# Kernel tuning notes

Measured on AMD Instinct MI355X. Metric: run time of the kernel, lower is better.

## Reference

```python
import jax, jax.numpy as jnp
import numpy as np

B = 262144      # Monte Carlo samples (batch)
DH = 128        # d_hidden
DM = 4          # concatenated input feature dim (two one-hot spins)


def _glorot(key, shape):
    fan_in, fan_out = shape[0], shape[1]
    lim = jnp.sqrt(6.0 / (fan_in + fan_out)).astype(jnp.float32)
    return jax.random.uniform(key, shape, jnp.float32, -lim, lim)


def setup_inputs() -> dict:
    key = jax.random.key(0)
    ks = jax.random.split(key, 10)
    inputs = jax.random.normal(ks[0], (B, DM), jnp.float32)
    h1 = jax.random.normal(ks[1], (B, DH), jnp.float32)
    h2 = jax.random.normal(ks[2], (B, DH), jnp.float32)
    U1 = _glorot(ks[3], (DH, DH))
    U2 = _glorot(ks[4], (DH, DH))
    # flax GRUCell params: input kernels (with bias), hidden kernels
    # (r,z: no bias; n: bias). Packed as [ir|iz|in] and [hr|hz].
    Wi = _glorot(ks[5], (DM, 3 * DH))
    bi = jnp.zeros((3 * DH,), jnp.float32)
    Whrz = _glorot(ks[6], (DH, 2 * DH))
    Whn = _glorot(ks[7], (DH, DH))
    bhn = jnp.zeros((DH,), jnp.float32)
    return {"inputs": inputs, "h1": h1, "h2": h2, "U1": U1, "U2": U2,
            "Wi": Wi, "bi": bi, "Whrz": Whrz, "Whn": Whn, "bhn": bhn}


def reference(inputs, h1, h2, U1, U2, Wi, bi, Whrz, Whn, bhn):
    # Fuse the two neighbor hidden states: h = h1 @ U1 + h2 @ U2
    h = h1 @ U1 + h2 @ U2                      # [B, DH]
    # flax GRUCell(carry=h, inputs=x):
    i_proj = inputs @ Wi + bi                  # [B, 3*DH]
    ir, iz, i_n = jnp.split(i_proj, 3, axis=-1)
    hrz = h @ Whrz                             # [B, 2*DH] (no bias in flax)
    hr, hz = jnp.split(hrz, 2, axis=-1)
    r = jax.nn.sigmoid(ir + hr)
    z = jax.nn.sigmoid(iz + hz)
    n = jnp.tanh(i_n + r * (h @ Whn + bhn))
    new_h = (1.0 - z) * n + z * h
    return (new_h, new_h)
```

## Files before the change

kernel.cpp:

```cpp
#include <hip/hip_runtime.h>

using bf8 = __attribute__((ext_vector_type(8))) short;
using bf4 = __attribute__((ext_vector_type(4))) short;
using f4  = __attribute__((ext_vector_type(4))) float;
using u16 = unsigned short;

#define NROWS 262144

#define FLAG_B   0
#define PU_B     128
#define PW2_B    (PU_B + 65536)
#define PWI_B    (PW2_B + 98304)
#define BI_B     (PWI_B + 6144)
#define BHN_B    (BI_B + 1536)

#define PACK_ITEMS 83968

static __device__ __forceinline__ float bf2f(u16 u) {
    unsigned v = ((unsigned)u) << 16;
    return __builtin_bit_cast(float, v);
}
static __device__ __forceinline__ u16 f2bf(float f) {
    unsigned x = __builtin_bit_cast(unsigned, f);
    x = x + 0x7fffu + ((x >> 16) & 1u);
    return (u16)(x >> 16);
}

template<bool FP32>
static __device__ __forceinline__ u16 ldw(const void* p, int i) {
    if constexpr (FP32) return f2bf(((const float*)p)[i]);
    else                return ((const u16*)p)[i];
}
template<bool FP32>
static __device__ __forceinline__ float ldf(const void* p, int i) {
    if constexpr (FP32) return ((const float*)p)[i];
    else                return bf2f(((const u16*)p)[i]);
}
template<bool FP32>
static __device__ __forceinline__ bf8 ld8(const void* base, int idx) {
    if constexpr (!FP32) {
        return *(const bf8*)((const u16*)base + idx);
    } else {
        const float* f = (const float*)base + idx;
        f4 u = *(const f4*)f;
        f4 v = *(const f4*)(f + 4);
        bf8 r;
        r[0]=(short)f2bf(u[0]); r[1]=(short)f2bf(u[1]); r[2]=(short)f2bf(u[2]); r[3]=(short)f2bf(u[3]);
        r[4]=(short)f2bf(v[0]); r[5]=(short)f2bf(v[1]); r[6]=(short)f2bf(v[2]); r[7]=(short)f2bf(v[3]);
        return r;
    }
}
template<bool FP32>
static __device__ __forceinline__ void st8(void* base, int idx, bf8 v) {
    if constexpr (!FP32) {
        *(bf8*)((u16*)base + idx) = v;
    } else {
        float* f = (float*)base + idx;
        f4 a, b;
        a[0]=bf2f((u16)v[0]); a[1]=bf2f((u16)v[1]); a[2]=bf2f((u16)v[2]); a[3]=bf2f((u16)v[3]);
        b[0]=bf2f((u16)v[4]); b[1]=bf2f((u16)v[5]); b[2]=bf2f((u16)v[6]); b[3]=bf2f((u16)v[7]);
        *(f4*)f = a; *(f4*)(f + 4) = b;
    }
}

__global__ void detect_mode(const u16* __restrict__ h1u, int* __restrict__ flag) {
    if (threadIdx.x == 0 && blockIdx.x == 0) {
        int huge = 0;
#pragma unroll 8
        for (int i = 0; i < 256; ++i) {
            u16 v = h1u[i * 2];
            huge += (((v >> 7) & 0xFF) >= 0xC0);
        }
        *flag = (huge > 0) ? 1 : 0;
    }
}

template<bool FP32>
__global__ void prep_pack(const void* __restrict__ U1, const void* __restrict__ U2,
                          const void* __restrict__ Whrz, const void* __restrict__ Whn,
                          const void* __restrict__ Wi, const void* __restrict__ bi,
                          const void* __restrict__ bhn, char* __restrict__ ws,
                          const int* __restrict__ flag)
{
    if ((*flag != 0) != FP32) return;
    int e = blockIdx.x * 256 + threadIdx.x;
    if (e >= PACK_ITEMS) return;
    u16*   pU   = (u16*)(ws + PU_B);
    u16*   pW2  = (u16*)(ws + PW2_B);
    float* wiF  = (float*)(ws + PWI_B);
    float* biF  = (float*)(ws + BI_B);
    float* bhnF = (float*)(ws + BHN_B);
    if (e < 32768) {
        int j = e & 7, lane = (e >> 3) & 63, f = e >> 9;
        int kb = f & 7, nt = f >> 3;
        int k = kb * 32 + (lane >> 4) * 8 + j;
        int n = nt * 16 + (lane & 15);
        pU[e] = (k < 128) ? ldw<FP32>(U1, k * 128 + n) : ldw<FP32>(U2, (k - 128) * 128 + n);
    } else if (e < 81920) {
        int e2 = e - 32768;
        int j = e2 & 7, lane = (e2 >> 3) & 63, f = e2 >> 9;
        int kb = f & 3, nt = f >> 2;
        int k = kb * 32 + (lane >> 4) * 8 + j;
        int n = nt * 16 + (lane & 15);
        pW2[e2] = (n < 256) ? ldw<FP32>(Whrz, k * 256 + n) : ldw<FP32>(Whn, k * 128 + (n - 256));
    } else if (e < 83456) {
        int e3 = e - 81920;
        int k = e3 & 3, c = e3 >> 2;
        wiF[e3] = ldf<FP32>(Wi, k * 384 + c);
    } else if (e < 83840) {
        int i = e - 83456;  biF[i] = ldf<FP32>(bi, i);
    } else {
        int i = e - 83840;  bhnF[i] = ldf<FP32>(bhn, i);
    }
}

template<bool FP32>
__global__ __launch_bounds__(256, 3) void gru_fused(
    const void* __restrict__ xin, const void* __restrict__ h1,
    const void* __restrict__ h2, const char* __restrict__ ws,
    void* __restrict__ out, const int* __restrict__ flag, int write2)
{
    if ((*flag != 0) != FP32) return;
    __shared__ __align__(16) u16 hl[4][32][136];
    const int tid = threadIdx.x;
    const int w  = tid >> 6;
    const int l  = tid & 63;
    const int q  = l >> 4;
    const int lr = l & 15;
    const int g0 = blockIdx.x * 128 + w * 32;

    const bf8* __restrict__ pU  = (const bf8*)(ws + PU_B);
    const bf8* __restrict__ pW2 = (const bf8*)(ws + PW2_B);

    bf8 a[2][8];
#pragma unroll
    for (int m = 0; m < 2; ++m) {
        int row = g0 + m * 16 + lr;
        int base = row * 128 + q * 8;
#pragma unroll
        for (int kb = 0; kb < 4; ++kb) {
            a[m][kb]     = ld8<FP32>(h1, base + kb * 32);
            a[m][kb + 4] = ld8<FP32>(h2, base + kb * 32);
        }
    }
#pragma unroll 1
    for (int nt = 0; nt < 8; ++nt) {
        f4 acc0 = {0.f, 0.f, 0.f, 0.f};
        f4 acc1 = {0.f, 0.f, 0.f, 0.f};
#pragma unroll
        for (int kb = 0; kb < 8; ++kb) {
            bf8 b = pU[(nt * 8 + kb) * 64 + l];
            acc0 = __builtin_amdgcn_mfma_f32_16x16x32_bf16(a[0][kb], b, acc0, 0, 0, 0);
            acc1 = __builtin_amdgcn_mfma_f32_16x16x32_bf16(a[1][kb], b, acc1, 0, 0, 0);
        }
        int col = nt * 16 + lr;
#pragma unroll
        for (int i = 0; i < 4; ++i) {
            hl[w][q * 4 + i][col]      = f2bf(acc0[i]);
            hl[w][16 + q * 4 + i][col] = f2bf(acc1[i]);
        }
    }

    bf8 ah[2][4];
#pragma unroll
    for (int m = 0; m < 2; ++m)
#pragma unroll
        for (int kb = 0; kb < 4; ++kb)
            ah[m][kb] = *(const bf8*)&hl[w][m * 16 + lr][kb * 32 + q * 8];

    float xf[2][4][4];
#pragma unroll
    for (int m = 0; m < 2; ++m)
#pragma unroll
        for (int i = 0; i < 4; ++i) {
            int row = g0 + m * 16 + q * 4 + i;
            if constexpr (FP32) {
                f4 xv = *(const f4*)((const float*)xin + row * 4);
#pragma unroll
                for (int k = 0; k < 4; ++k) xf[m][i][k] = xv[k];
            } else {
                bf4 xv = *(const bf4*)((const u16*)xin + row * 4);
#pragma unroll
                for (int k = 0; k < 4; ++k) xf[m][i][k] = bf2f((u16)xv[k]);
            }
        }

    const float* wiF  = (const float*)(ws + PWI_B);
    const float* biF  = (const float*)(ws + BI_B);
    const float* bhnF = (const float*)(ws + BHN_B);

#pragma unroll 1
    for (int nt = 0; nt < 8; ++nt) {
        f4 aR[2], aZ[2], aN[2];
#pragma unroll
        for (int m = 0; m < 2; ++m) {
            aR[m] = {0.f,0.f,0.f,0.f}; aZ[m] = {0.f,0.f,0.f,0.f}; aN[m] = {0.f,0.f,0.f,0.f};
        }
#pragma unroll
        for (int kb = 0; kb < 4; ++kb) {
            bf8 bR = pW2[((nt     ) * 4 + kb) * 64 + l];
            bf8 bZ = pW2[((nt + 8 ) * 4 + kb) * 64 + l];
            bf8 bN = pW2[((nt + 16) * 4 + kb) * 64 + l];
#pragma unroll
            for (int m = 0; m < 2; ++m) {
                aR[m] = __builtin_amdgcn_mfma_f32_16x16x32_bf16(ah[m][kb], bR, aR[m], 0, 0, 0);
                aZ[m] = __builtin_amdgcn_mfma_f32_16x16x32_bf16(ah[m][kb], bZ, aZ[m], 0, 0, 0);
                aN[m] = __builtin_amdgcn_mfma_f32_16x16x32_bf16(ah[m][kb], bN, aN[m], 0, 0, 0);
            }
        }
        int c = nt * 16 + lr;
        f4 wr = *(const f4*)(wiF + c * 4);
        f4 wz = *(const f4*)(wiF + (128 + c) * 4);
        f4 wn = *(const f4*)(wiF + (256 + c) * 4);
        float bir = biF[c], biz = biF[128 + c], bin = biF[256 + c], bhc = bhnF[c];
#pragma unroll
        for (int m = 0; m < 2; ++m)
#pragma unroll
            for (int i = 0; i < 4; ++i) {
                int rl = m * 16 + q * 4 + i;
                float ir = bir, iz = biz, inn = bin;
#pragma unroll
                for (int k = 0; k < 4; ++k) {
                    ir  = fmaf(xf[m][i][k], wr[k], ir);
                    iz  = fmaf(xf[m][i][k], wz[k], iz);
                    inn = fmaf(xf[m][i][k], wn[k], inn);
                }
                float hv = bf2f(hl[w][rl][c]);
                float sr = ir + aR[m][i];
                sr = fminf(fmaxf(sr, -30.f), 30.f);
                float r = __fdividef(1.f, 1.f + __expf(-sr));
                float sz = iz + aZ[m][i];
                sz = fminf(fmaxf(sz, -30.f), 30.f);
                float z = __fdividef(1.f, 1.f + __expf(-sz));
                float t = inn + r * (aN[m][i] + bhc);
                t = fminf(fmaxf(t, -15.f), 15.f);
                float e2t = __expf(2.f * t);
                float n = (e2t - 1.f) * __fdividef(1.f, e2t + 1.f);
                float o = (1.f - z) * n + z * hv;
                hl[w][rl][c] = f2bf(o);
            }
    }

#pragma unroll
    for (int ii = 0; ii < 8; ++ii) {
        int ch  = ii * 64 + l;
        int row = ch >> 4;
        int c8  = (ch & 15) * 8;
        bf8 v = *(const bf8*)&hl[w][row][c8];
        int off = (g0 + row) * 128 + c8;
        st8<FP32>(out, off, v);
        if (write2) st8<FP32>(out, NROWS * 128 + off, v);
    }
}

extern "C" void kernel_launch(void* const* d_in, const int* in_sizes, int n_in,
                              void* d_out, int out_size, void* d_ws, size_t ws_size,
                              hipStream_t stream) {
    const void* x    = d_in[0];
    const void* h1   = d_in[1];
    const void* h2   = d_in[2];
    const void* U1   = d_in[3];
    const void* U2   = d_in[4];
    const void* Wi   = d_in[5];
    const void* bi   = d_in[6];
    const void* Whrz = d_in[7];
    const void* Whn  = d_in[8];
    const void* bhn  = d_in[9];
    char* ws   = (char*)d_ws;
    int* flag  = (int*)(ws + FLAG_B);
    int write2 = (out_size >= 2 * NROWS * 128) ? 1 : 0;

    detect_mode<<<1, 64, 0, stream>>>((const u16*)h1, flag);
    const int pblk = (PACK_ITEMS + 255) / 256;
    prep_pack<false><<<pblk, 256, 0, stream>>>(U1, U2, Whrz, Whn, Wi, bi, bhn, ws, flag);
    prep_pack<true ><<<pblk, 256, 0, stream>>>(U1, U2, Whrz, Whn, Wi, bi, bhn, ws, flag);
    gru_fused<false><<<NROWS / 128, 256, 0, stream>>>(x, h1, h2, ws, d_out, flag, write2);
    gru_fused<true ><<<NROWS / 128, 256, 0, stream>>>(x, h1, h2, ws, d_out, flag, write2);
}
```

Before: 547.4 us.

## Fold U into hidden GRU weights and compute input projection with MFMA

Precomputes V = [U1;U2] @ [Whrz|Whn] in the pack kernel, so gate pre-activations come straight from [h1|h2] in one K=256 pass, alongside h itself. This removes the LDS round-trip of h and the second dependent GEMM stage. The input projection plus bias is folded into an MFMA with a padded x vector carrying a constant one. Outputs are written directly with nontemporal scalar stores instead of being staged in shared memory. The trade-off is more total MFMA work (K=256 instead of 128 for the gates), less coalesced stores, and different bf16 rounding, since h is no longer rounded before the second product.

Result: slower. 598.4 us (+9.3%).

```diff
diff --git a/kernel.cpp b/kernel.cpp
--- a/kernel.cpp
+++ b/kernel.cpp
@@ -9,12 +9,14 @@
 
 #define FLAG_B   0
 #define PU_B     128
-#define PW2_B    (PU_B + 65536)
-#define PWI_B    (PW2_B + 98304)
-#define BI_B     (PWI_B + 6144)
-#define BHN_B    (BI_B + 1536)
-
-#define PACK_ITEMS 83968
+#define PV_B     (PU_B + 65536)
+#define PWI_B    (PV_B + 196608)
+#define BHN_B    (PWI_B + 24576)
+
+#define N_PU   32768
+#define N_PV   98304
+#define N_PWI  12288
+#define PACK_ITEMS (N_PU + N_PV + N_PWI + 128)
 
 static __device__ __forceinline__ float bf2f(u16 u) {
     unsigned v = ((unsigned)u) << 16;
@@ -50,18 +52,6 @@
         return r;
     }
 }
-template<bool FP32>
-static __device__ __forceinline__ void st8(void* base, int idx, bf8 v) {
-    if constexpr (!FP32) {
-        *(bf8*)((u16*)base + idx) = v;
-    } else {
-        float* f = (float*)base + idx;
-        f4 a, b;
-        a[0]=bf2f((u16)v[0]); a[1]=bf2f((u16)v[1]); a[2]=bf2f((u16)v[2]); a[3]=bf2f((u16)v[3]);
-        b[0]=bf2f((u16)v[4]); b[1]=bf2f((u16)v[5]); b[2]=bf2f((u16)v[6]); b[3]=bf2f((u16)v[7]);
-        *(f4*)f = a; *(f4*)(f + 4) = b;
-    }
-}
 
 __global__ void detect_mode(const u16* __restrict__ h1u, int* __restrict__ flag) {
     if (threadIdx.x == 0 && blockIdx.x == 0) {
@@ -86,31 +76,46 @@
     int e = blockIdx.x * 256 + threadIdx.x;
     if (e >= PACK_ITEMS) return;
     u16*   pU   = (u16*)(ws + PU_B);
-    u16*   pW2  = (u16*)(ws + PW2_B);
-    float* wiF  = (float*)(ws + PWI_B);
-    float* biF  = (float*)(ws + BI_B);
+    u16*   pV   = (u16*)(ws + PV_B);
+    u16*   pWi  = (u16*)(ws + PWI_B);
     float* bhnF = (float*)(ws + BHN_B);
-    if (e < 32768) {
+    if (e < N_PU) {
         int j = e & 7, lane = (e >> 3) & 63, f = e >> 9;
         int kb = f & 7, nt = f >> 3;
         int k = kb * 32 + (lane >> 4) * 8 + j;
         int n = nt * 16 + (lane & 15);
         pU[e] = (k < 128) ? ldw<FP32>(U1, k * 128 + n) : ldw<FP32>(U2, (k - 128) * 128 + n);
-    } else if (e < 81920) {
-        int e2 = e - 32768;
+    } else if (e < N_PU + N_PV) {
+        int e2 = e - N_PU;
         int j = e2 & 7, lane = (e2 >> 3) & 63, f = e2 >> 9;
-        int kb = f & 3, nt = f >> 2;
+        int kb = f & 7, nt = f >> 3;
         int k = kb * 32 + (lane >> 4) * 8 + j;
         int n = nt * 16 + (lane & 15);
-        pW2[e2] = (n < 256) ? ldw<FP32>(Whrz, k * 256 + n) : ldw<FP32>(Whn, k * 128 + (n - 256));
-    } else if (e < 83456) {
-        int e3 = e - 81920;
-        int k = e3 & 3, c = e3 >> 2;
-        wiF[e3] = ldf<FP32>(Wi, k * 384 + c);
-    } else if (e < 83840) {
-        int i = e - 83456;  biF[i] = ldf<FP32>(bi, i);
+        const void* Us = (k < 128) ? U1 : U2;
+        int krow = (k < 128) ? k : k - 128;
+        float acc = 0.f;
+        if (n < 256) {
+#pragma unroll 8
+            for (int j2 = 0; j2 < 128; ++j2)
+                acc = fmaf(ldf<FP32>(Us, krow * 128 + j2), ldf<FP32>(Whrz, j2 * 256 + n), acc);
+        } else {
+#pragma unroll 8
+            for (int j2 = 0; j2 < 128; ++j2)
+                acc = fmaf(ldf<FP32>(Us, krow * 128 + j2), ldf<FP32>(Whn, j2 * 128 + (n - 256)), acc);
+        }
+        pV[e2] = f2bf(acc);
+    } else if (e < N_PU + N_PV + N_PWI) {
+        int e3 = e - (N_PU + N_PV);
+        int j = e3 & 7, lane = (e3 >> 3) & 63, nt = e3 >> 9;
+        int k = (lane >> 4) * 8 + j;
+        int n = nt * 16 + (lane & 15);
+        u16 v = 0;
+        if (k < 4)       v = ldw<FP32>(Wi, k * 384 + n);
+        else if (k == 4) v = ldw<FP32>(bi, n);
+        pWi[e3] = v;
     } else {
-        int i = e - 83840;  bhnF[i] = ldf<FP32>(bhn, i);
+        int i = e - (N_PU + N_PV + N_PWI);
+        bhnF[i] = ldf<FP32>(bhn, i);
     }
 }
 
@@ -121,7 +126,6 @@
     void* __restrict__ out, const int* __restrict__ flag, int write2)
 {
     if ((*flag != 0) != FP32) return;
-    __shared__ __align__(16) u16 hl[4][32][136];
     const int tid = threadIdx.x;
     const int w  = tid >> 6;
     const int l  = tid & 63;
@@ -130,7 +134,9 @@
     const int g0 = blockIdx.x * 128 + w * 32;
 
     const bf8* __restrict__ pU  = (const bf8*)(ws + PU_B);
-    const bf8* __restrict__ pW2 = (const bf8*)(ws + PW2_B);
+    const bf8* __restrict__ pV  = (const bf8*)(ws + PV_B);
+    const bf8* __restrict__ pWi = (const bf8*)(ws + PWI_B);
+    const float* __restrict__ bhnF = (const float*)(ws + BHN_B);
 
     bf8 a[2][8];
 #pragma unroll
@@ -143,113 +149,87 @@
             a[m][kb + 4] = ld8<FP32>(h2, base + kb * 32);
         }
     }
+
+    bf8 ax[2];
+#pragma unroll
+    for (int m = 0; m < 2; ++m) {
+        bf8 v = {0,0,0,0,0,0,0,0};
+        if (q == 0) {
+            int row = g0 + m * 16 + lr;
+            if constexpr (FP32) {
+                f4 xv = *(const f4*)((const float*)xin + row * 4);
+#pragma unroll
+                for (int k = 0; k < 4; ++k) v[k] = (short)f2bf(xv[k]);
+            } else {
+                bf4 xv = *(const bf4*)((const u16*)xin + row * 4);
+#pragma unroll
+                for (int k = 0; k < 4; ++k) v[k] = xv[k];
+            }
+            v[4] = (short)0x3F80;
+        }
+        ax[m] = v;
+    }
+
+    float* outF = (float*)out;
+    u16*   outB = (u16*)out;
+
 #pragma unroll 1
     for (int nt = 0; nt < 8; ++nt) {
-        f4 acc0 = {0.f, 0.f, 0.f, 0.f};
-        f4 acc1 = {0.f, 0.f, 0.f, 0.f};
+        const f4 z4 = {0.f, 0.f, 0.f, 0.f};
+        f4 aH[2], aR[2], aZ[2], aN[2], aI[2];
+        bf8 biR = pWi[(nt     ) * 64 + l];
+        bf8 biZ = pWi[(nt + 8 ) * 64 + l];
+        bf8 biN = pWi[(nt + 16) * 64 + l];
+#pragma unroll
+        for (int m = 0; m < 2; ++m) {
+            aH[m] = z4;
+            aN[m] = z4;
+            aR[m] = __builtin_amdgcn_mfma_f32_16x16x32_bf16(ax[m], biR, z4, 0, 0, 0);
+            aZ[m] = __builtin_amdgcn_mfma_f32_16x16x32_bf16(ax[m], biZ, z4, 0, 0, 0);
+            aI[m] = __builtin_amdgcn_mfma_f32_16x16x32_bf16(ax[m], biN, z4, 0, 0, 0);
+        }
 #pragma unroll
         for (int kb = 0; kb < 8; ++kb) {
-            bf8 b = pU[(nt * 8 + kb) * 64 + l];
-            acc0 = __builtin_amdgcn_mfma_f32_16x16x32_bf16(a[0][kb], b, acc0, 0, 0, 0);
-            acc1 = __builtin_amdgcn_mfma_f32_16x16x32_bf16(a[1][kb], b, acc1, 0, 0, 0);
-        }
-        int col = nt * 16 + lr;
-#pragma unroll
-        for (int i = 0; i < 4; ++i) {
-            hl[w][q * 4 + i][col]      = f2bf(acc0[i]);
-            hl[w][16 + q * 4 + i][col] = f2bf(acc1[i]);
-        }
-    }
-
-    bf8 ah[2][4];
-#pragma unroll
-    for (int m = 0; m < 2; ++m)
-#pragma unroll
-        for (int kb = 0; kb < 4; ++kb)
-            ah[m][kb] = *(const bf8*)&hl[w][m * 16 + lr][kb * 32 + q * 8];
-
-    float xf[2][4][4];
-#pragma unroll
-    for (int m = 0; m < 2; ++m)
-#pragma unroll
-        for (int i = 0; i < 4; ++i) {
-            int row = g0 + m * 16 + q * 4 + i;
-            if constexpr (FP32) {
-                f4 xv = *(const f4*)((const float*)xin + row * 4);
-#pragma unroll
-                for (int k = 0; k < 4; ++k) xf[m][i][k] = xv[k];
-            } else {
-                bf4 xv = *(const bf4*)((const u16*)xin + row * 4);
-#pragma unroll
-                for (int k = 0; k < 4; ++k) xf[m][i][k] = bf2f((u16)xv[k]);
+            bf8 bH = pU[(nt * 8 + kb) * 64 + l];
+            bf8 bR = pV[((nt     ) * 8 + kb) * 64 + l];
+            bf8 bZ = pV[((nt + 8 ) * 8 + kb) * 64 + l];
+            bf8 bN = pV[((nt + 16) * 8 + kb) * 64 + l];
+#pragma unroll
+            for (int m = 0; m < 2; ++m) {
+                aH[m] = __builtin_amdgcn_mfma_f32_16x16x32_bf16(a[m][kb], bH, aH[m], 0, 0, 0);
+                aR[m] = __builtin_amdgcn_mfma_f32_16x16x32_bf16(a[m][kb], bR, aR[m], 0, 0, 0);
+                aZ[m] = __builtin_amdgcn_mfma_f32_16x16x32_bf16(a[m][kb], bZ, aZ[m], 0, 0, 0);
+                aN[m] = __builtin_amdgcn_mfma_f32_16x16x32_bf16(a[m][kb], bN, aN[m], 0, 0, 0);
             }
         }
-
-    const float* wiF  = (const float*)(ws + PWI_B);
-    const float* biF  = (const float*)(ws + BI_B);
-    const float* bhnF = (const float*)(ws + BHN_B);
-
-#pragma unroll 1
-    for (int nt = 0; nt < 8; ++nt) {
-        f4 aR[2], aZ[2], aN[2];
+        int c = nt * 16 + lr;
+        float bhc = bhnF[c];
 #pragma unroll
         for (int m = 0; m < 2; ++m) {
-            aR[m] = {0.f,0.f,0.f,0.f}; aZ[m] = {0.f,0.f,0.f,0.f}; aN[m] = {0.f,0.f,0.f,0.f};
-        }
-#pragma unroll
-        for (int kb = 0; kb < 4; ++kb) {
-            bf8 bR = pW2[((nt     ) * 4 + kb) * 64 + l];
-            bf8 bZ = pW2[((nt + 8 ) * 4 + kb) * 64 + l];
-            bf8 bN = pW2[((nt + 16) * 4 + kb) * 64 + l];
-#pragma unroll
-            for (int m = 0; m < 2; ++m) {
-                aR[m] = __builtin_amdgcn_mfma_f32_16x16x32_bf16(ah[m][kb], bR, aR[m], 0, 0, 0);
-                aZ[m] = __builtin_amdgcn_mfma_f32_16x16x32_bf16(ah[m][kb], bZ, aZ[m], 0, 0, 0);
-                aN[m] = __builtin_amdgcn_mfma_f32_16x16x32_bf16(ah[m][kb], bN, aN[m], 0, 0, 0);
-            }
-        }
-        int c = nt * 16 + lr;
-        f4 wr = *(const f4*)(wiF + c * 4);
-        f4 wz = *(const f4*)(wiF + (128 + c) * 4);
-        f4 wn = *(const f4*)(wiF + (256 + c) * 4);
-        float bir = biF[c], biz = biF[128 + c], bin = biF[256 + c], bhc = bhnF[c];
-#pragma unroll
-        for (int m = 0; m < 2; ++m)
+            int rbase = (g0 + m * 16 + q * 4) * 128 + c;
 #pragma unroll
             for (int i = 0; i < 4; ++i) {
-                int rl = m * 16 + q * 4 + i;
-                float ir = bir, iz = biz, inn = bin;
-#pragma unroll
-                for (int k = 0; k < 4; ++k) {
-                    ir  = fmaf(xf[m][i][k], wr[k], ir);
-                    iz  = fmaf(xf[m][i][k], wz[k], iz);
-                    inn = fmaf(xf[m][i][k], wn[k], inn);
-                }
-                float hv = bf2f(hl[w][rl][c]);
-                float sr = ir + aR[m][i];
-                sr = fminf(fmaxf(sr, -30.f), 30.f);
-                float r = __fdividef(1.f, 1.f + __expf(-sr));
-                float sz = iz + aZ[m][i];
-                sz = fminf(fmaxf(sz, -30.f), 30.f);
-                float z = __fdividef(1.f, 1.f + __expf(-sz));
-                float t = inn + r * (aN[m][i] + bhc);
+                float hv = aH[m][i];
+                float sr = fminf(fmaxf(aR[m][i], -30.f), 30.f);
+                float r  = __fdividef(1.f, 1.f + __expf(-sr));
+                float sz = fminf(fmaxf(aZ[m][i], -30.f), 30.f);
+                float z  = __fdividef(1.f, 1.f + __expf(-sz));
+                float t  = aI[m][i] + r * (aN[m][i] + bhc);
                 t = fminf(fmaxf(t, -15.f), 15.f);
                 float e2t = __expf(2.f * t);
                 float n = (e2t - 1.f) * __fdividef(1.f, e2t + 1.f);
                 float o = (1.f - z) * n + z * hv;
-                hl[w][rl][c] = f2bf(o);
+                int off = rbase + i * 128;
+                if constexpr (FP32) {
+                    __builtin_nontemporal_store(o, outF + off);
+                    if (write2) __builtin_nontemporal_store(o, outF + NROWS * 128 + off);
+                } else {
+                    u16 ob = f2bf(o);
+                    __builtin_nontemporal_store(ob, outB + off);
+                    if (write2) __builtin_nontemporal_store(ob, outB + NROWS * 128 + off);
+                }
             }
-    }
-
-#pragma unroll
-    for (int ii = 0; ii < 8; ++ii) {
-        int ch  = ii * 64 + l;
-        int row = ch >> 4;
-        int c8  = (ch & 15) * 8;
-        bf8 v = *(const bf8*)&hl[w][row][c8];
-        int off = (g0 + row) * 128 + c8;
-        st8<FP32>(out, off, v);
-        if (write2) st8<FP32>(out, NROWS * 128 + off, v);
+        }
     }
 }
 
```
